# Optimization experiments

Hardware: AMD Instinct MI355X
Metric: run time of the kernel (lower is better)

The kernel has to match this reference:

```python
import jax, jax.numpy as jnp
import numpy as np

N_NODES = 50000
N_EDGES = 800000
D_IN = 128
D_HID = 128
D_OUT = 128


def setup_inputs() -> dict:
    key = jax.random.key(0)
    ks = jax.random.split(key, 12)
    features = jax.random.normal(ks[0], (N_NODES, D_IN), dtype=jnp.float32)
    src = jax.random.randint(ks[1], (N_EDGES,), 0, N_NODES, dtype=jnp.int32)
    dst = jax.random.randint(ks[2], (N_EDGES,), 0, N_NODES, dtype=jnp.int32)
    s_in = 1.0 / np.sqrt(D_IN)
    s_hid = 1.0 / np.sqrt(D_HID)
    W1 = jax.random.normal(ks[3], (D_IN, D_HID), dtype=jnp.float32) * s_in
    b1 = jnp.zeros((D_HID,), dtype=jnp.float32)
    W2 = jax.random.normal(ks[4], (D_HID, D_HID), dtype=jnp.float32) * s_hid
    b2 = jnp.zeros((D_HID,), dtype=jnp.float32)
    W3 = jax.random.normal(ks[5], (D_HID, D_OUT), dtype=jnp.float32) * s_hid
    b3 = jnp.zeros((D_OUT,), dtype=jnp.float32)
    policy_w = jax.random.normal(ks[6], (D_OUT, 1), dtype=jnp.float32) * s_hid
    policy_b = jnp.zeros((1,), dtype=jnp.float32)
    value_w = jax.random.normal(ks[7], (D_OUT, 1), dtype=jnp.float32) * s_hid
    value_b = jnp.zeros((1,), dtype=jnp.float32)
    return {
        "features": features, "src": src, "dst": dst,
        "W1": W1, "b1": b1, "W2": W2, "b2": b2, "W3": W3, "b3": b3,
        "policy_w": policy_w, "policy_b": policy_b,
        "value_w": value_w, "value_b": value_b,
    }


def _graph_conv(h, src, dst, deg_inv, W, b, act):
    # DGL GraphConv with norm='left': scale source features by 1/out_degree,
    # sum messages over incoming edges, then linear transform + bias (+ act).
    hn = h * deg_inv  # [N, d]
    agg = jax.ops.segment_sum(hn[src], dst, num_segments=N_NODES)  # SpMM: [N, d]
    out = agg @ W + b
    return jax.nn.relu(out) if act else out


def reference(features, src, dst, W1, b1, W2, b2, W3, b3,
              policy_w, policy_b, value_w, value_b):
    ones = jnp.ones((src.shape[0],), dtype=features.dtype)
    deg = jax.ops.segment_sum(ones, src, num_segments=N_NODES)  # out-degree
    deg_inv = (1.0 / jnp.clip(deg, 1.0))[:, None]  # [N, 1]

    h = _graph_conv(features, src, dst, deg_inv, W1, b1, act=True)
    h = _graph_conv(h, src, dst, deg_inv, W2, b2, act=True)
    h = _graph_conv(h, src, dst, deg_inv, W3, b3, act=False)  # last layer: no activation

    mN = jnp.mean(h, axis=0, keepdims=True)  # mean readout over nodes, [1, D_OUT]
    PI = h @ policy_w + policy_b  # [N, 1]
    V = mN @ value_w + value_b    # [1, 1]
    return PI, V
```

## Files before the change

kernel.cpp:

```cpp
#include <hip/hip_runtime.h>


#define N_NODES 50000
#define N_EDGES 800000
#define D 128
#define NSH 8
#define PANEL ((size_t)N_NODES * 16)
#define NC 64
#define CSZ (N_EDGES / NC)
#define NW (N_NODES / 2)


__global__ __launch_bounds__(512) void k_hist3(const int* __restrict__ src, const int* __restrict__ dst,
                                               unsigned* __restrict__ ghd16, unsigned* __restrict__ ghs16) {
    __shared__ unsigned h[NW];
    const int arr = blockIdx.x & 1;
    const int c   = blockIdx.x >> 1;
    const int t = threadIdx.x;
    for (int i = t; i < NW; i += 512) h[i] = 0u;
    __syncthreads();
    const int* __restrict__ col = arr ? src : dst;
    const int e0 = c * CSZ, e1 = e0 + CSZ;
    for (int e = e0 + t; e < e1; e += 512) {
        int n = col[e];
        atomicAdd(&h[n >> 1], 1u << ((n & 1) << 4));
    }
    __syncthreads();
    unsigned* __restrict__ outp = (arr ? ghs16 : ghd16) + (size_t)c * NW;
    for (int i = t; i < NW; i += 512) outp[i] = h[i];
}

__global__ __launch_bounds__(256) void k_merge3(unsigned* __restrict__ ghd16, const unsigned* __restrict__ ghs16,
                                                int* __restrict__ rowcnt, float* __restrict__ dinv) {
    int w = blockIdx.x * 256 + threadIdx.x;
    if (w >= NW) return;
    unsigned runlo = 0, runhi = 0;
#pragma unroll
    for (int c = 0; c < NC; c++) {
        unsigned v = ghd16[(size_t)c * NW + w];
        ghd16[(size_t)c * NW + w] = runlo | (runhi << 16);
        runlo += v & 0xffffu; runhi += v >> 16;
    }
    rowcnt[2 * w] = (int)runlo;
    rowcnt[2 * w + 1] = (int)runhi;
    unsigned dlo = 0, dhi = 0;
#pragma unroll
    for (int c = 0; c < NC; c++) {
        unsigned v = ghs16[(size_t)c * NW + w];
        dlo += v & 0xffffu; dhi += v >> 16;
    }
    dinv[2 * w]     = 1.0f / (float)(dlo > 1u ? dlo : 1u);
    dinv[2 * w + 1] = 1.0f / (float)(dhi > 1u ? dhi : 1u);
}

__global__ __launch_bounds__(1024) void k_scan1(const int* __restrict__ cnt, int* __restrict__ excl,
                                                int* __restrict__ blocksum, int n) {
    __shared__ int wsum[16];
    int i = blockIdx.x * 1024 + threadIdx.x;
    int v = (i < n) ? cnt[i] : 0;
    int lane = threadIdx.x & 63, wid = threadIdx.x >> 6;
    int x = v;
#pragma unroll
    for (int off = 1; off < 64; off <<= 1) {
        int y = __shfl_up(x, off, 64);
        if (lane >= off) x += y;
    }
    if (lane == 63) wsum[wid] = x;
    __syncthreads();
    if (threadIdx.x == 0) {
        int run = 0;
        for (int w = 0; w < 16; w++) { int t = wsum[w]; wsum[w] = run; run += t; }
        blocksum[blockIdx.x] = run;
    }
    __syncthreads();
    if (i < n) excl[i] = (x - v) + wsum[wid];
}

__global__ void k_scan2(const int* __restrict__ blocksum, int* __restrict__ blockoff,
                        int* __restrict__ rowptr_last, int nblk) {
    if (threadIdx.x == 0) {
        int run = 0;
        for (int b = 0; b < nblk; b++) { int t = blocksum[b]; blockoff[b] = run; run += t; }
        rowptr_last[0] = run;
    }
}

__global__ __launch_bounds__(1024) void k_scan3(int* __restrict__ excl, const int* __restrict__ blockoff, int n) {
    int i = blockIdx.x * 1024 + threadIdx.x;
    if (i < n) excl[i] += blockoff[blockIdx.x];
}

__global__ __launch_bounds__(512) void k_fill3(const int* __restrict__ src, const int* __restrict__ dst,
                                               const int* __restrict__ rowptr, const unsigned* __restrict__ ghd16,
                                               int* __restrict__ csrc) {
    __shared__ unsigned cnt[NW];
    const int c = blockIdx.x;
    const int t = threadIdx.x;
    for (int i = t; i < NW; i += 512) cnt[i] = 0u;
    __syncthreads();
    const unsigned* __restrict__ basep = ghd16 + (size_t)c * NW;
    const int e0 = c * CSZ, e1 = e0 + CSZ;
    for (int e = e0 + t; e < e1; e += 512) {
        int d = dst[e];
        int sh = (d & 1) << 4;
        unsigned old = atomicAdd(&cnt[d >> 1], 1u << sh);
        int p = (int)((old >> sh) & 0xffffu);
        int base = (int)((basep[d >> 1] >> sh) & 0xffffu);
        csrc[rowptr[d] + base + p] = src[e];
    }
}


__global__ __launch_bounds__(256) void k_panelize(const float* __restrict__ in, const float* __restrict__ dinv,
                                                  float* __restrict__ outp) {
    int tid = blockIdx.x * 256 + threadIdx.x;
    if (tid >= N_NODES * 32) return;
    int p = tid / (N_NODES * 4);
    int r = tid - p * (N_NODES * 4);
    int node = r >> 2, qq = r & 3;
    float w = dinv[node];
    float4 v = *reinterpret_cast<const float4*>(&in[(size_t)node * D + p * 16 + qq * 4]);
    v.x *= w; v.y *= w; v.z *= w; v.w *= w;
    *reinterpret_cast<float4*>(&outp[(size_t)p * PANEL + (size_t)node * 16 + qq * 4]) = v;
}


__global__ __launch_bounds__(256) void k_agg(const float* __restrict__ hp,
                                             const int* __restrict__ rp, const int* __restrict__ csrc,
                                             float* __restrict__ outp) {
    const int l4 = threadIdx.x & 3;
    const int grp = threadIdx.x >> 2;
    const int slice = blockIdx.x & (NSH - 1);
    const int node = (blockIdx.x >> 3) * 64 + grp;
    if (node >= N_NODES) return;
    const float* __restrict__ pan = hp + (size_t)slice * PANEL + l4 * 4;
    int s0 = rp[node], s1 = rp[node + 1];
    float4 acc = {0.f, 0.f, 0.f, 0.f};
    int e = s0;
    int npre = (s0 + 3) & ~3; if (npre > s1) npre = s1;
    for (; e < npre; e++) {
        float4 a = *reinterpret_cast<const float4*>(&pan[(size_t)csrc[e] * 16]);
        acc.x += a.x; acc.y += a.y; acc.z += a.z; acc.w += a.w;
    }
    for (; e + 4 <= s1; e += 4) {
        int4 ii = *reinterpret_cast<const int4*>(&csrc[e]);
        float4 a = *reinterpret_cast<const float4*>(&pan[(size_t)ii.x * 16]);
        float4 b = *reinterpret_cast<const float4*>(&pan[(size_t)ii.y * 16]);
        float4 c = *reinterpret_cast<const float4*>(&pan[(size_t)ii.z * 16]);
        float4 d = *reinterpret_cast<const float4*>(&pan[(size_t)ii.w * 16]);
        acc.x += (a.x + b.x) + (c.x + d.x);
        acc.y += (a.y + b.y) + (c.y + d.y);
        acc.z += (a.z + b.z) + (c.z + d.z);
        acc.w += (a.w + b.w) + (c.w + d.w);
    }
    for (; e < s1; e++) {
        float4 a = *reinterpret_cast<const float4*>(&pan[(size_t)csrc[e] * 16]);
        acc.x += a.x; acc.y += a.y; acc.z += a.z; acc.w += a.w;
    }
    *reinterpret_cast<float4*>(&outp[(size_t)slice * PANEL + (size_t)node * 16 + l4 * 4]) = acc;
}


__global__ __launch_bounds__(256) void k_gemm(const float* __restrict__ in, const float* __restrict__ W,
                                              const float* __restrict__ bias, float* __restrict__ out,
                                              int nrows, int relu,
                                              const float* __restrict__ dscale,
                                              const float* __restrict__ pw, const float* __restrict__ pb,
                                              float* __restrict__ pi_out, float* __restrict__ colsum) {
    __shared__ float wl[D * D];
    __shared__ float at[D * 32];
    int t = threadIdx.x;
    const int head = (pw != nullptr);
    for (int i = t; i < D * D / 4; i += 256)
        reinterpret_cast<float4*>(wl)[i] = reinterpret_cast<const float4*>(W)[i];
    const int tx = t & 31;
    const int ty = t >> 5;
    const int ldrow = t & 31;
    const int ldc   = t >> 5;
    float4 bv = reinterpret_cast<const float4*>(bias)[tx];
    float4 pwv = head ? reinterpret_cast<const float4*>(pw)[tx] : float4{0.f, 0.f, 0.f, 0.f};
    float pb0 = head ? pb[0] : 0.f;
    const int op = tx >> 2, oq = tx & 3;
    float cs0 = 0.f, cs1 = 0.f, cs2 = 0.f, cs3 = 0.f;
    int ntiles = (nrows + 31) / 32;

    for (int tile = blockIdx.x; tile < ntiles; tile += gridDim.x) {
        int row0 = tile * 32;
        __syncthreads();
        {
            int gr = row0 + ldrow;
            float va[16];
            if (gr < nrows) {
                const float4* ap = reinterpret_cast<const float4*>(&in[(size_t)ldc * PANEL + (size_t)gr * 16]);
#pragma unroll
                for (int qq = 0; qq < 4; qq++) {
                    float4 v = ap[qq];
                    va[qq * 4 + 0] = v.x; va[qq * 4 + 1] = v.y;
                    va[qq * 4 + 2] = v.z; va[qq * 4 + 3] = v.w;
                }
            } else {
#pragma unroll
                for (int qq = 0; qq < 16; qq++) va[qq] = 0.f;
            }
            int kb = ldc * 16;
#pragma unroll
            for (int j = 0; j < 16; j++) at[(kb + j) * 32 + ldrow] = va[j];
        }
        __syncthreads();

        float acc[4][4];
#pragma unroll
        for (int j = 0; j < 4; j++)
#pragma unroll
            for (int c = 0; c < 4; c++) acc[j][c] = 0.f;

#pragma unroll 8
        for (int k = 0; k < D; k++) {
            float4 a = *reinterpret_cast<const float4*>(&at[k * 32 + ty * 4]);
            float4 w = *reinterpret_cast<const float4*>(&wl[k * D + tx * 4]);
            acc[0][0] += a.x * w.x; acc[0][1] += a.x * w.y; acc[0][2] += a.x * w.z; acc[0][3] += a.x * w.w;
            acc[1][0] += a.y * w.x; acc[1][1] += a.y * w.y; acc[1][2] += a.y * w.z; acc[1][3] += a.y * w.w;
            acc[2][0] += a.z * w.x; acc[2][1] += a.z * w.y; acc[2][2] += a.z * w.z; acc[2][3] += a.z * w.w;
            acc[3][0] += a.w * w.x; acc[3][1] += a.w * w.y; acc[3][2] += a.w * w.z; acc[3][3] += a.w * w.w;
        }

#pragma unroll
        for (int j = 0; j < 4; j++) {
            int gr = row0 + ty * 4 + j;
            if (gr < nrows) {
                float4 o;
                o.x = acc[j][0] + bv.x; o.y = acc[j][1] + bv.y;
                o.z = acc[j][2] + bv.z; o.w = acc[j][3] + bv.w;
                if (relu) {
                    o.x = fmaxf(o.x, 0.f); o.y = fmaxf(o.y, 0.f);
                    o.z = fmaxf(o.z, 0.f); o.w = fmaxf(o.w, 0.f);
                }
                if (head) {
                    cs0 += o.x; cs1 += o.y; cs2 += o.z; cs3 += o.w;
                    float pr = o.x * pwv.x + o.y * pwv.y + o.z * pwv.z + o.w * pwv.w;
#pragma unroll
                    for (int off = 16; off > 0; off >>= 1) pr += __shfl_xor(pr, off, 32);
                    if (tx == 0) pi_out[gr] = pr + pb0;
                } else {
                    if (dscale) {
                        float w = dscale[gr];
                        o.x *= w; o.y *= w; o.z *= w; o.w *= w;
                    }
                    *reinterpret_cast<float4*>(&out[(size_t)op * PANEL + (size_t)gr * 16 + oq * 4]) = o;
                }
            }
        }
    }

    if (head) {
        __syncthreads();
        float* csl = at;
        if (t < D) csl[t] = 0.f;
        __syncthreads();
        atomicAdd(&csl[tx * 4 + 0], cs0);
        atomicAdd(&csl[tx * 4 + 1], cs1);
        atomicAdd(&csl[tx * 4 + 2], cs2);
        atomicAdd(&csl[tx * 4 + 3], cs3);
        __syncthreads();
        if (t < D) atomicAdd(&colsum[t], csl[t]);
    }
}


__global__ __launch_bounds__(128) void k_value(const float* __restrict__ colsum, const float* __restrict__ vw,
                                               const float* __restrict__ vb, float* __restrict__ out) {
    __shared__ float red[128];
    int t = threadIdx.x;
    red[t] = (colsum[t] * (1.0f / (float)N_NODES)) * vw[t];
    __syncthreads();
    for (int s = 64; s > 0; s >>= 1) {
        if (t < s) red[t] += red[t + s];
        __syncthreads();
    }
    if (t == 0) out[0] = red[0] + vb[0];
}

__global__ __launch_bounds__(64) void k_ws_too_small(float* __restrict__ out, int n) {
    int i = blockIdx.x * 64 + threadIdx.x;
    if (i < n) out[i] = -1e30f;
}


extern "C" void kernel_launch(void* const* d_in, const int* in_sizes, int n_in,
                              void* d_out, int out_size, void* d_ws, size_t ws_size,
                              hipStream_t stream) {
    const float* features = (const float*)d_in[0];
    const int*   src      = (const int*)d_in[1];
    const int*   dst      = (const int*)d_in[2];
    const float* W1 = (const float*)d_in[3];
    const float* b1 = (const float*)d_in[4];
    const float* W2 = (const float*)d_in[5];
    const float* b2 = (const float*)d_in[6];
    const float* W3 = (const float*)d_in[7];
    const float* b3 = (const float*)d_in[8];
    const float* pw = (const float*)d_in[9];
    const float* pb = (const float*)d_in[10];
    const float* vw = (const float*)d_in[11];
    const float* vb = (const float*)d_in[12];
    float* out = (float*)d_out;

    char* ws = (char*)d_ws;
    size_t off = 0;
    auto alloc = [&](size_t bytes) -> char* {
        char* p = ws + off;
        off += (bytes + 255) & ~(size_t)255;
        return p;
    };
    float* dinv     = (float*)alloc((size_t)N_NODES * 4);
    int*   rowptr   = (int*)alloc((size_t)(N_NODES + 1) * 4);
    int*   blocksum = (int*)alloc(64 * 4);
    int*   blockoff = (int*)alloc(64 * 4);
    float* colsum   = (float*)alloc(D * 4);
    int*   csrc     = (int*)alloc((size_t)N_EDGES * 4);
    float* bufA     = (float*)alloc((size_t)N_NODES * D * 4);
    float* bufB     = (float*)alloc((size_t)N_NODES * D * 4);

    unsigned* ghd16 = (unsigned*)bufB;
    unsigned* ghs16 = ghd16 + (size_t)NC * NW;
    int* rowcnt     = (int*)(ghs16 + (size_t)NC * NW);

    if (off > ws_size) {
        k_ws_too_small<<<(out_size + 63) / 64, 64, 0, stream>>>(out, out_size);
        return;
    }

    hipMemsetAsync(colsum, 0, (size_t)D * 4, stream);

    k_hist3<<<2 * NC, 512, 0, stream>>>(src, dst, ghd16, ghs16);
    k_merge3<<<(NW + 255) / 256, 256, 0, stream>>>(ghd16, ghs16, rowcnt, dinv);

    int nblk = (N_NODES + 1023) / 1024;
    k_scan1<<<nblk, 1024, 0, stream>>>(rowcnt, rowptr, blocksum, N_NODES);
    k_scan2<<<1, 64, 0, stream>>>(blocksum, blockoff, rowptr + N_NODES, nblk);
    k_scan3<<<nblk, 1024, 0, stream>>>(rowptr, blockoff, N_NODES);
    k_fill3<<<NC, 512, 0, stream>>>(src, dst, rowptr, ghd16, csrc);

    k_panelize<<<(N_NODES * 32 + 255) / 256, 256, 0, stream>>>(features, dinv, bufA);

    int aggblocks = ((N_NODES + 63) / 64) * NSH;
    k_agg<<<aggblocks, 256, 0, stream>>>(bufA, rowptr, csrc, bufB);
    k_gemm<<<512, 256, 0, stream>>>(bufB, W1, b1, bufB, N_NODES, 1, dinv,
                                    nullptr, nullptr, nullptr, nullptr);
    k_agg<<<aggblocks, 256, 0, stream>>>(bufB, rowptr, csrc, bufA);
    k_gemm<<<512, 256, 0, stream>>>(bufA, W2, b2, bufA, N_NODES, 1, dinv,
                                    nullptr, nullptr, nullptr, nullptr);
    k_agg<<<aggblocks, 256, 0, stream>>>(bufA, rowptr, csrc, bufB);
    k_gemm<<<512, 256, 0, stream>>>(bufB, W3, b3, nullptr, N_NODES, 0, nullptr,
                                    pw, pb, out, colsum);

    k_value<<<1, 128, 0, stream>>>(colsum, vw, vb, out + N_NODES);
}
```

Before: 341.7 us.

## Use 16-bit CSR indices padded to multiples of eight for aggregation

Source indices in the CSR are stored as unsigned short, since the node count fits in 16 bits. Each row is padded to a multiple of eight entries that point at an added all-zero panel row. The aggregation kernel then loads eight indices with one 16-byte read and gathers eight rows per iteration, with no prologue or tail loops. This halves index traffic and raises memory-level parallelism. In exchange it adds a padding kernel and extra gathers of the zero row, and it only works while the node count stays below 65536.

```diff
diff --git a/kernel.cpp b/kernel.cpp
--- a/kernel.cpp
+++ b/kernel.cpp
@@ -5,10 +5,12 @@
 #define N_EDGES 800000
 #define D 128
 #define NSH 8
-#define PANEL ((size_t)N_NODES * 16)
+#define PROWS (N_NODES + 8)
+#define PANEL ((size_t)PROWS * 16)
 #define NC 64
 #define CSZ (N_EDGES / NC)
 #define NW (N_NODES / 2)
+#define CS_CAP (N_EDGES + 8 * N_NODES)
 
 
 __global__ __launch_bounds__(512) void k_hist3(const int* __restrict__ src, const int* __restrict__ dst,
@@ -31,7 +33,8 @@
 }
 
 __global__ __launch_bounds__(256) void k_merge3(unsigned* __restrict__ ghd16, const unsigned* __restrict__ ghs16,
-                                                int* __restrict__ rowcnt, float* __restrict__ dinv) {
+                                                int* __restrict__ rowcnt, int* __restrict__ rowtrue,
+                                                float* __restrict__ dinv) {
     int w = blockIdx.x * 256 + threadIdx.x;
     if (w >= NW) return;
     unsigned runlo = 0, runhi = 0;
@@ -41,8 +44,10 @@
         ghd16[(size_t)c * NW + w] = runlo | (runhi << 16);
         runlo += v & 0xffffu; runhi += v >> 16;
     }
-    rowcnt[2 * w] = (int)runlo;
-    rowcnt[2 * w + 1] = (int)runhi;
+    rowtrue[2 * w]     = (int)runlo;
+    rowtrue[2 * w + 1] = (int)runhi;
+    rowcnt[2 * w]      = (int)((runlo + 7u) & ~7u);
+    rowcnt[2 * w + 1]  = (int)((runhi + 7u) & ~7u);
     unsigned dlo = 0, dhi = 0;
 #pragma unroll
     for (int c = 0; c < NC; c++) {
@@ -92,7 +97,7 @@
 
 __global__ __launch_bounds__(512) void k_fill3(const int* __restrict__ src, const int* __restrict__ dst,
                                                const int* __restrict__ rowptr, const unsigned* __restrict__ ghd16,
-                                               int* __restrict__ csrc) {
+                                               unsigned short* __restrict__ cs16) {
     __shared__ unsigned cnt[NW];
     const int c = blockIdx.x;
     const int t = threadIdx.x;
@@ -106,7 +111,23 @@
         unsigned old = atomicAdd(&cnt[d >> 1], 1u << sh);
         int p = (int)((old >> sh) & 0xffffu);
         int base = (int)((basep[d >> 1] >> sh) & 0xffffu);
-        csrc[rowptr[d] + base + p] = src[e];
+        cs16[rowptr[d] + base + p] = (unsigned short)src[e];
+    }
+}
+
+__global__ __launch_bounds__(256) void k_pad(const int* __restrict__ rowptr, const int* __restrict__ rowtrue,
+                                             unsigned short* __restrict__ cs16,
+                                             float* __restrict__ bufA, float* __restrict__ bufB) {
+    int n = blockIdx.x * 256 + threadIdx.x;
+    if (n < N_NODES) {
+        int e0 = rowptr[n] + rowtrue[n], e1 = rowptr[n + 1];
+        for (int e = e0; e < e1; e++) cs16[e] = (unsigned short)N_NODES;
+    }
+    if (blockIdx.x == 0) {
+        int t = threadIdx.x;
+        float* b = (t & 128) ? bufB : bufA;
+        int p = (t >> 4) & 7, cc = t & 15;
+        b[(size_t)p * PANEL + (size_t)N_NODES * 16 + cc] = 0.f;
     }
 }
 
@@ -126,7 +147,7 @@
 
 
 __global__ __launch_bounds__(256) void k_agg(const float* __restrict__ hp,
-                                             const int* __restrict__ rp, const int* __restrict__ csrc,
+                                             const int* __restrict__ rp, const unsigned short* __restrict__ cs16,
                                              float* __restrict__ outp) {
     const int l4 = threadIdx.x & 3;
     const int grp = threadIdx.x >> 2;
@@ -136,26 +157,24 @@
     const float* __restrict__ pan = hp + (size_t)slice * PANEL + l4 * 4;
     int s0 = rp[node], s1 = rp[node + 1];
     float4 acc = {0.f, 0.f, 0.f, 0.f};
-    int e = s0;
-    int npre = (s0 + 3) & ~3; if (npre > s1) npre = s1;
-    for (; e < npre; e++) {
-        float4 a = *reinterpret_cast<const float4*>(&pan[(size_t)csrc[e] * 16]);
-        acc.x += a.x; acc.y += a.y; acc.z += a.z; acc.w += a.w;
-    }
-    for (; e + 4 <= s1; e += 4) {
-        int4 ii = *reinterpret_cast<const int4*>(&csrc[e]);
-        float4 a = *reinterpret_cast<const float4*>(&pan[(size_t)ii.x * 16]);
-        float4 b = *reinterpret_cast<const float4*>(&pan[(size_t)ii.y * 16]);
-        float4 c = *reinterpret_cast<const float4*>(&pan[(size_t)ii.z * 16]);
-        float4 d = *reinterpret_cast<const float4*>(&pan[(size_t)ii.w * 16]);
-        acc.x += (a.x + b.x) + (c.x + d.x);
-        acc.y += (a.y + b.y) + (c.y + d.y);
-        acc.z += (a.z + b.z) + (c.z + d.z);
-        acc.w += (a.w + b.w) + (c.w + d.w);
-    }
-    for (; e < s1; e++) {
-        float4 a = *reinterpret_cast<const float4*>(&pan[(size_t)csrc[e] * 16]);
-        acc.x += a.x; acc.y += a.y; acc.z += a.z; acc.w += a.w;
+    for (int e = s0; e < s1; e += 8) {
+        int4 r = *reinterpret_cast<const int4*>(&cs16[e]);
+        int i0 = r.x & 0xffff, i1 = (r.x >> 16) & 0xffff;
+        int i2 = r.y & 0xffff, i3 = (r.y >> 16) & 0xffff;
+        int i4 = r.z & 0xffff, i5 = (r.z >> 16) & 0xffff;
+        int i6 = r.w & 0xffff, i7 = (r.w >> 16) & 0xffff;
+        float4 a0 = *reinterpret_cast<const float4*>(&pan[(size_t)i0 * 16]);
+        float4 a1 = *reinterpret_cast<const float4*>(&pan[(size_t)i1 * 16]);
+        float4 a2 = *reinterpret_cast<const float4*>(&pan[(size_t)i2 * 16]);
+        float4 a3 = *reinterpret_cast<const float4*>(&pan[(size_t)i3 * 16]);
+        float4 a4 = *reinterpret_cast<const float4*>(&pan[(size_t)i4 * 16]);
+        float4 a5 = *reinterpret_cast<const float4*>(&pan[(size_t)i5 * 16]);
+        float4 a6 = *reinterpret_cast<const float4*>(&pan[(size_t)i6 * 16]);
+        float4 a7 = *reinterpret_cast<const float4*>(&pan[(size_t)i7 * 16]);
+        acc.x += ((a0.x + a1.x) + (a2.x + a3.x)) + ((a4.x + a5.x) + (a6.x + a7.x));
+        acc.y += ((a0.y + a1.y) + (a2.y + a3.y)) + ((a4.y + a5.y) + (a6.y + a7.y));
+        acc.z += ((a0.z + a1.z) + (a2.z + a3.z)) + ((a4.z + a5.z) + (a6.z + a7.z));
+        acc.w += ((a0.w + a1.w) + (a2.w + a3.w)) + ((a4.w + a5.w) + (a6.w + a7.w));
     }
     *reinterpret_cast<float4*>(&outp[(size_t)slice * PANEL + (size_t)node * 16 + l4 * 4]) = acc;
 }
@@ -313,16 +332,17 @@
     };
     float* dinv     = (float*)alloc((size_t)N_NODES * 4);
     int*   rowptr   = (int*)alloc((size_t)(N_NODES + 1) * 4);
+    int*   rowcnt   = (int*)alloc((size_t)N_NODES * 4);
+    int*   rowtrue  = (int*)alloc((size_t)N_NODES * 4);
     int*   blocksum = (int*)alloc(64 * 4);
     int*   blockoff = (int*)alloc(64 * 4);
     float* colsum   = (float*)alloc(D * 4);
-    int*   csrc     = (int*)alloc((size_t)N_EDGES * 4);
-    float* bufA     = (float*)alloc((size_t)N_NODES * D * 4);
-    float* bufB     = (float*)alloc((size_t)N_NODES * D * 4);
+    unsigned short* cs16 = (unsigned short*)alloc((size_t)CS_CAP * 2);
+    float* bufA     = (float*)alloc((size_t)NSH * PANEL * 4);
+    float* bufB     = (float*)alloc((size_t)NSH * PANEL * 4);
 
     unsigned* ghd16 = (unsigned*)bufB;
     unsigned* ghs16 = ghd16 + (size_t)NC * NW;
-    int* rowcnt     = (int*)(ghs16 + (size_t)NC * NW);
 
     if (off > ws_size) {
         k_ws_too_small<<<(out_size + 63) / 64, 64, 0, stream>>>(out, out_size);
@@ -332,24 +352,25 @@
     hipMemsetAsync(colsum, 0, (size_t)D * 4, stream);
 
     k_hist3<<<2 * NC, 512, 0, stream>>>(src, dst, ghd16, ghs16);
-    k_merge3<<<(NW + 255) / 256, 256, 0, stream>>>(ghd16, ghs16, rowcnt, dinv);
+    k_merge3<<<(NW + 255) / 256, 256, 0, stream>>>(ghd16, ghs16, rowcnt, rowtrue, dinv);
 
     int nblk = (N_NODES + 1023) / 1024;
     k_scan1<<<nblk, 1024, 0, stream>>>(rowcnt, rowptr, blocksum, N_NODES);
     k_scan2<<<1, 64, 0, stream>>>(blocksum, blockoff, rowptr + N_NODES, nblk);
     k_scan3<<<nblk, 1024, 0, stream>>>(rowptr, blockoff, N_NODES);
-    k_fill3<<<NC, 512, 0, stream>>>(src, dst, rowptr, ghd16, csrc);
+    k_fill3<<<NC, 512, 0, stream>>>(src, dst, rowptr, ghd16, cs16);
+    k_pad<<<(N_NODES + 255) / 256, 256, 0, stream>>>(rowptr, rowtrue, cs16, bufA, bufB);
 
     k_panelize<<<(N_NODES * 32 + 255) / 256, 256, 0, stream>>>(features, dinv, bufA);
 
     int aggblocks = ((N_NODES + 63) / 64) * NSH;
-    k_agg<<<aggblocks, 256, 0, stream>>>(bufA, rowptr, csrc, bufB);
+    k_agg<<<aggblocks, 256, 0, stream>>>(bufA, rowptr, cs16, bufB);
     k_gemm<<<512, 256, 0, stream>>>(bufB, W1, b1, bufB, N_NODES, 1, dinv,
                                     nullptr, nullptr, nullptr, nullptr);
-    k_agg<<<aggblocks, 256, 0, stream>>>(bufB, rowptr, csrc, bufA);
+    k_agg<<<aggblocks, 256, 0, stream>>>(bufB, rowptr, cs16, bufA);
     k_gemm<<<512, 256, 0, stream>>>(bufA, W2, b2, bufA, N_NODES, 1, dinv,
                                     nullptr, nullptr, nullptr, nullptr);
-    k_agg<<<aggblocks, 256, 0, stream>>>(bufA, rowptr, csrc, bufB);
+    k_agg<<<aggblocks, 256, 0, stream>>>(bufA, rowptr, cs16, bufB);
     k_gemm<<<512, 256, 0, stream>>>(bufB, W3, b3, nullptr, N_NODES, 0, nullptr,
                                     pw, pb, out, colsum);
 
```

New measurement: 309.7 us. 1.1x faster.
